# Kernel tuning notes

Hardware: AMD Instinct MI355X
Metric: run time of the kernel (lower is better)

The kernel has to match this reference:

```python
import jax, jax.numpy as jnp
import numpy as np

N, FIN, C1, C2 = 4096, 6, 1000, 1000
K1, K2, KR = 3, 6, 3
NR, S, NCLS = 20, 205, 40


def pairwise_adj(x):
    # exp(-squared_euclidean_distance), RGCNN pairwise_distance
    inner = -2.0 * jnp.einsum('bnf,bmf->bnm', x, x)
    sq = jnp.sum(x * x, axis=-1, keepdims=True)
    return jnp.exp(-(sq + inner + jnp.swapaxes(sq, 1, 2)))


def knn_sparsify(adj, k):
    # keep top-k similarities per row, zero the rest (get_one_matrix_knn)
    vals, idx = jax.lax.top_k(adj, k)
    B, n, _ = adj.shape
    b = jnp.arange(B)[:, None, None]
    r = jnp.arange(n)[None, :, None]
    return jnp.zeros_like(adj).at[b, r, idx].set(vals)


def get_laplacian(W):
    # normalized Laplacian L = I - D^-1/2 W D^-1/2
    dinv = 1.0 / jnp.sqrt(jnp.sum(W, axis=-1))
    Lnorm = W * dinv[:, :, None] * dinv[:, None, :]
    return jnp.eye(W.shape[-1], dtype=W.dtype)[None] - Lnorm


def cheb_conv(x, L, W, b, K):
    # Chebyshev recursion: Tx0=x, Tx1=Lx, Txk=2L Tx_{k-1} - Tx_{k-2}
    Tx = [x]
    if K > 1:
        Tx.append(jnp.einsum('bnm,bmf->bnf', L, x))
    for _ in range(2, K):
        Tx.append(2.0 * jnp.einsum('bnm,bmf->bnf', L, Tx[-1]) - Tx[-2])
    xhat = jnp.concatenate(Tx, axis=-1)  # [B, N, K*Fin]
    return jnp.einsum('bnf,fo->bno', xhat, W) + b


def setup_inputs() -> dict:
    key = jax.random.key(0)
    ks = jax.random.split(key, 16)
    sc = 0.02
    return {
        'x': jax.random.normal(ks[0], (1, N, FIN), jnp.float32),
        'k': 40,
        'batch_size': 1,
        'num_points': N,
        'vertices_Reeb': jax.random.normal(ks[1], (NR, 3), jnp.float32),
        'laplacian_Reeb': jax.random.normal(ks[2], (NR, NR), jnp.float32),
        'sccs': jax.random.randint(ks[3], (NR, S), 0, N),
        'W1': jax.random.normal(ks[4], (K1 * FIN, C1), jnp.float32) * sc,
        'b1': jnp.zeros((C1,), jnp.float32),
        'W2': jax.random.normal(ks[5], (K2 * C1, C2), jnp.float32) * sc,
        'b2': jnp.zeros((C2,), jnp.float32),
        'Wr': jax.random.normal(ks[6], (KR * C1, C2), jnp.float32) * sc,
        'br': jnp.zeros((C2,), jnp.float32),
        'fc1_w': jax.random.normal(ks[7], (2 * C2, 512), jnp.float32) * sc,
        'fc1_b': jnp.zeros((512,), jnp.float32),
        'fc2_w': jax.random.normal(ks[8], (512, 128), jnp.float32) * sc,
        'fc2_b': jnp.zeros((128,), jnp.float32),
        'fc3_w': jax.random.normal(ks[9], (128, NCLS), jnp.float32) * sc,
        'fc3_b': jnp.zeros((NCLS,), jnp.float32),
    }


def reference(x, k, batch_size, num_points, vertices_Reeb, laplacian_Reeb, sccs,
              W1, b1, W2, b2, Wr, br, fc1_w, fc1_b, fc2_w, fc2_b, fc3_w, fc3_b):
    fro = lambda a: jnp.linalg.norm(a.reshape(-1))
    regs = []
    # dynamic KNN graph + Laplacian (no_grad in original -> stop_gradient)
    L = jax.lax.stop_gradient(get_laplacian(knn_sparsify(pairwise_adj(x), k)))
    out = jax.nn.relu(cheb_conv(x, L, W1, b1, K1))  # [1, N, 1000]
    regs.append(fro(jnp.einsum('bnc,bnm,bmf->bcf', out, L, x)))
    # Reeb pooling: max over each scc's node features (sample 0)
    vfr = jnp.max(out[0][sccs], axis=1)[None]  # [1, 20, 1000]
    L_reeb = laplacian_Reeb[None]
    # second dynamic graph on features
    L2 = jax.lax.stop_gradient(get_laplacian(knn_sparsify(pairwise_adj(out), k)))
    out2 = jax.nn.relu(cheb_conv(out, L2, W2, b2, K2))
    regs.append(fro(jnp.einsum('bnc,bnm,bmf->bcf', out2, L2, x)))
    out_reeb = jax.nn.relu(cheb_conv(vfr, L_reeb, Wr, br, KR))
    out_m = jnp.max(out2, axis=1)       # [1, 1000]
    reeb_m = jnp.max(out_reeb, axis=1)  # [1, 1000]
    of = jnp.concatenate([reeb_m, out_m], axis=1)  # [1, 2000]
    of = jax.nn.relu(of @ fc1_w + fc1_b)
    regs += [jnp.linalg.norm(fc1_w.T[0]) ** 2, fc1_b[0] ** 2]
    of = jax.nn.relu(of @ fc2_w + fc2_b)
    regs += [jnp.linalg.norm(fc2_w.T[0]) ** 2, fc2_b[0] ** 2]
    of = of @ fc3_w + fc3_b  # [1, 40]
    regs += [jnp.linalg.norm(fc3_w.T[0]) ** 2, fc3_b[0] ** 2]
    return of, jnp.stack(regs)
```

## Files before the change

### kernel.cpp

```cpp
#include <hip/hip_runtime.h>
#include <math.h>

#define N4    4096
#define FDIM  6
#define CC    1000
#define KP    1024
#define KP6   (6 * KP)
#define KNN   40
#define NRB   20
#define SSC   205

typedef __attribute__((ext_vector_type(8))) short bf16x8;
typedef __attribute__((ext_vector_type(4))) float f32x4;

__device__ __forceinline__ unsigned short f2bf(float f) {
    unsigned u = __float_as_uint(f);
    u = (u + 0x7fffu + ((u >> 16) & 1u)) >> 16;
    return (unsigned short)u;
}
__device__ __forceinline__ float bf2f(short s) {
    return __uint_as_float(((unsigned)(unsigned short)s) << 16);
}

__device__ __forceinline__ unsigned d2key(float d) {
    unsigned u = __float_as_uint(d);
    return ((int)u < 0) ? u : (~u) ^ 0x80000000u;
}
__device__ __forceinline__ float key2d(unsigned k) {
    unsigned u = (k >> 31) ? k : (~k) ^ 0x80000000u;
    return __uint_as_float(u);
}

__device__ __forceinline__ void gload16(const unsigned short* g, short* l) {
    __builtin_amdgcn_global_load_lds(
        (const __attribute__((address_space(1))) unsigned int*)g,
        (__attribute__((address_space(3))) unsigned int*)l, 16, 0, 0);
}


__global__ __launch_bounds__(256) void sqx_kernel(const float* __restrict__ x,
                                                  float* __restrict__ sq1,
                                                  float* __restrict__ xhat) {
    int n = blockIdx.x * blockDim.x + threadIdx.x;
    if (n >= N4) return;
    float s = 0.f;
#pragma unroll
    for (int f = 0; f < FDIM; ++f) {
        float v = x[n * FDIM + f];
        s += v * v;
        xhat[n * 18 + f] = v;
    }
    sq1[n] = s;
}


#define NHC 8
#define HSTRIDE 257

struct TopkSh {
    unsigned sv[N4];
    int hist[NHC * HSTRIDE];
    int sc[256];
    float red[8];
    unsigned short cidx[N4];
    unsigned s_pfx;
    int s_need, s_cnt, s_m;
};

__device__ __forceinline__ void hist_pick(TopkSh& sh, int level, int t, int lane, int w, int nc) {
    if (t < 256) {
        int cnt = 0;
        for (int c = 0; c < nc; ++c) cnt += sh.hist[c * HSTRIDE + t];
        sh.sc[t] = cnt;
    }
    __syncthreads();
    if (w == 0) {
        int need = sh.s_need;
        unsigned pfx = sh.s_pfx;
        int c0 = sh.sc[4 * lane + 0], c1 = sh.sc[4 * lane + 1];
        int c2 = sh.sc[4 * lane + 2], c3 = sh.sc[4 * lane + 3];
        int s = c0 + c1 + c2 + c3;
        int suf = s;
#pragma unroll
        for (int off = 1; off < 64; off <<= 1) {
            int ov = __shfl_down(suf, off, 64);
            if (lane + off < 64) suf += ov;
        }
        int above = suf - s;
        int i3 = above + c3, i2 = i3 + c2, i1 = i2 + c1, i0 = i1 + c0;
        if (i3 >= need && i3 - c3 < need) { sh.s_need = need - (i3 - c3); sh.s_pfx = pfx | ((unsigned)(4 * lane + 3) << level); }
        if (i2 >= need && i2 - c2 < need) { sh.s_need = need - (i2 - c2); sh.s_pfx = pfx | ((unsigned)(4 * lane + 2) << level); }
        if (i1 >= need && i1 - c1 < need) { sh.s_need = need - (i1 - c1); sh.s_pfx = pfx | ((unsigned)(4 * lane + 1) << level); }
        if (i0 >= need && i0 - c0 < need) { sh.s_need = need - (i0 - c0); sh.s_pfx = pfx | ((unsigned)(4 * lane + 0) << level); }
    }
    __syncthreads();
}

__device__ void topk_select(TopkSh& sh, int n, int* __restrict__ idx,
                            float* __restrict__ val, float* __restrict__ rowsum) {
    int t = threadIdx.x, lane = t & 63, w = t >> 6;
    if (t == 0) { sh.s_pfx = 0u; sh.s_need = KNN; sh.s_cnt = 0; sh.s_m = 0; }
    for (int q = t; q < NHC * HSTRIDE; q += 512) sh.hist[q] = 0;
    __syncthreads();
    int* hw = &sh.hist[(t & 7) * HSTRIDE];

    {
        unsigned prevb = 0xFFFFFFFFu; int rl = 0;
        for (int i = t; i < N4; i += 512) {
            unsigned b = sh.sv[i] >> 24;
            if (b == prevb) ++rl;
            else { if (rl) atomicAdd(&hw[prevb], rl); prevb = b; rl = 1; }
        }
        if (rl) atomicAdd(&hw[prevb], rl);
    }
    __syncthreads();
    hist_pick(sh, 24, t, lane, w, NHC);
    unsigned b1 = sh.s_pfx >> 24;

    for (int i = t; i < N4; i += 512) {
        unsigned u = sh.sv[i];
        bool isc = ((u >> 24) >= b1);
        unsigned long long mm = __ballot(isc);
        int cw = __popcll(mm);
        int base = 0;
        if (lane == 0 && cw) base = atomicAdd(&sh.s_m, cw);
        base = __shfl(base, 0);
        if (isc) sh.cidx[base + __popcll(mm & ((1ull << lane) - 1ull))] = (unsigned short)i;
    }
    __syncthreads();
    int mcnt = sh.s_m;

    for (int level = 16; level >= 0; level -= 8) {
        for (int q = t; q < HSTRIDE; q += 512) sh.hist[q] = 0;
        __syncthreads();
        unsigned pfx = sh.s_pfx;
        for (int j = t; j < mcnt; j += 512) {
            unsigned u = sh.sv[sh.cidx[j]];
            if ((u >> (level + 8)) == (pfx >> (level + 8)))
                atomicAdd(&sh.hist[(u >> level) & 255], 1);
        }
        __syncthreads();
        hist_pick(sh, level, t, lane, w, 1);
    }
    unsigned Tbits = sh.s_pfx;
    float Tf = __expf(-key2d(Tbits));
    int needEq = sh.s_need;

    float psum = 0.f;
    for (int j = t; j < mcnt; j += 512) {
        unsigned u = sh.sv[sh.cidx[j]];
        if (u > Tbits) {
            int p = atomicAdd(&sh.s_cnt, 1);
            float v = __expf(-key2d(u));
            idx[(size_t)n * KNN + p] = (int)sh.cidx[j];
            val[(size_t)n * KNN + p] = v;
            psum += v;
        }
    }
#pragma unroll
    for (int o = 32; o; o >>= 1) psum += __shfl_down(psum, o);
    if (lane == 0) sh.red[w] = psum;
    __syncthreads();
    if (t == 0) {
        float s = 0.f;
#pragma unroll
        for (int q = 0; q < 8; ++q) s += sh.red[q];
        rowsum[n] = s + (float)needEq * Tf;
    }

    if (t < 64) {
        int filled = KNN - needEq;
        for (int ib = 0; ib < N4 && filled < KNN; ib += 64) {
            bool eq = (sh.sv[ib + t] == Tbits);
            unsigned long long m = __ballot(eq);
            int pre = __popcll(m & ((1ull << t) - 1ull));
            if (eq && (filled + pre) < KNN) {
                idx[(size_t)n * KNN + filled + pre] = ib + t;
                val[(size_t)n * KNN + filled + pre] = Tf;
            }
            filled += __popcll(m);
        }
    }
}

__global__ __launch_bounds__(512) void topk_fused1(const float* __restrict__ x,
                                                   const float* __restrict__ sq1,
                                                   int* __restrict__ idx, float* __restrict__ val,
                                                   float* __restrict__ rowsum) {
    __shared__ TopkSh sh;
    __shared__ float xn[FDIM];
    __shared__ float sns;
    int n = blockIdx.x;
    int t = threadIdx.x;
    if (t < FDIM) xn[t] = x[n * FDIM + t];
    if (t == FDIM) sns = sq1[n];
    __syncthreads();
    float x0 = xn[0], x1 = xn[1], x2 = xn[2], x3 = xn[3], x4 = xn[4], x5 = xn[5];
    float sn = sns;
    for (int i = t; i < N4; i += 512) {
        const float2* xi = (const float2*)(x + i * FDIM);
        float2 p0 = xi[0], p1 = xi[1], p2 = xi[2];
        float d = x0 * p0.x + x1 * p0.y + x2 * p1.x + x3 * p1.y + x4 * p2.x + x5 * p2.y;
        float e = sn + sq1[i] - 2.f * d;
        sh.sv[i] = d2key(e);
    }
    topk_select(sh, n, idx, val, rowsum);
}

__global__ __launch_bounds__(512) void topk_radix(const unsigned short* __restrict__ S,
                                                  int* __restrict__ idx, float* __restrict__ val,
                                                  float* __restrict__ rowsum) {
    __shared__ TopkSh sh;
    int n = blockIdx.x;
    int t = threadIdx.x;
    const unsigned short* row = S + (size_t)n * N4;
    bf16x8 a = *(const bf16x8*)(row + 8 * t);
#pragma unroll
    for (int q = 0; q < 8; ++q) sh.sv[8 * t + q] = d2key(bf2f(a[q]));
    topk_select(sh, n, idx, val, rowsum);
}

__global__ __launch_bounds__(256) void wnorm_kernel(float* __restrict__ wv,
                                                    const int* __restrict__ idx,
                                                    const float* __restrict__ rs) {
    int i = blockIdx.x * 256 + threadIdx.x;
    if (i >= N4 * KNN) return;
    int n = i / KNN;
    wv[i] = wv[i] * rsqrtf(rs[n]) * rsqrtf(rs[idx[i]]);
}

__global__ __launch_bounds__(64) void spmv_cheb(const float* __restrict__ Tc,
                                                const float* __restrict__ Tp,
                                                float* __restrict__ Tn,
                                                const int* __restrict__ idx,
                                                const float* __restrict__ wv,
                                                int F, int sC, int sP, int sN,
                                                float a, float b) {
    __shared__ int   si[KNN];
    __shared__ float sw[KNN];
    int n = blockIdx.x;
    if (threadIdx.x < KNN) {
        si[threadIdx.x] = idx[(size_t)n * KNN + threadIdx.x];
        sw[threadIdx.x] = wv[(size_t)n * KNN + threadIdx.x];
    }
    __syncthreads();
    for (int c = threadIdx.x; c < F; c += blockDim.x) {
        float s = 0.f;
#pragma unroll 8
        for (int j = 0; j < KNN; ++j) s += sw[j] * Tc[(size_t)si[j] * sC + c];
        float v = a * (Tc[(size_t)n * sC + c] - s);
        if (b != 0.f) v -= b * Tp[(size_t)n * sP + c];
        Tn[(size_t)n * sN + c] = v;
    }
}

__global__ __launch_bounds__(256) void spmv_cheb_bf(const unsigned short* __restrict__ Tcbf,
                                                    const unsigned short* __restrict__ Tpbf,
                                                    unsigned short* __restrict__ Tnbf,
                                                    const int* __restrict__ idx,
                                                    const float* __restrict__ wv,
                                                    float a, float b) {
    __shared__ int   si[KNN];
    __shared__ float sw[KNN];
    __shared__ float part[128][8];
    int n = blockIdx.x;
    int t = threadIdx.x;
    int tt = t & 127, h = t >> 7;
    if (t < KNN) {
        si[t] = idx[(size_t)n * KNN + t];
        sw[t] = wv[(size_t)n * KNN + t];
    }
    __syncthreads();
    int c = tt * 8;
    float acc0 = 0, acc1 = 0, acc2 = 0, acc3 = 0, acc4 = 0, acc5 = 0, acc6 = 0, acc7 = 0;
    int j0 = h * 20;
#pragma unroll 4
    for (int j = j0; j < j0 + 20; ++j) {
        bf16x8 v = *(const bf16x8*)(Tcbf + (size_t)si[j] * KP6 + c);
        float wj = sw[j];
        acc0 += wj * bf2f(v[0]); acc1 += wj * bf2f(v[1]);
        acc2 += wj * bf2f(v[2]); acc3 += wj * bf2f(v[3]);
        acc4 += wj * bf2f(v[4]); acc5 += wj * bf2f(v[5]);
        acc6 += wj * bf2f(v[6]); acc7 += wj * bf2f(v[7]);
    }
    if (h == 1) {
        part[tt][0] = acc0; part[tt][1] = acc1; part[tt][2] = acc2; part[tt][3] = acc3;
        part[tt][4] = acc4; part[tt][5] = acc5; part[tt][6] = acc6; part[tt][7] = acc7;
    }
    __syncthreads();
    if (h == 0) {
        acc0 += part[tt][0]; acc1 += part[tt][1]; acc2 += part[tt][2]; acc3 += part[tt][3];
        acc4 += part[tt][4]; acc5 += part[tt][5]; acc6 += part[tt][6]; acc7 += part[tt][7];
        bf16x8 tc = *(const bf16x8*)(Tcbf + (size_t)n * KP6 + c);
        float o0 = a * (bf2f(tc[0]) - acc0), o1 = a * (bf2f(tc[1]) - acc1);
        float o2 = a * (bf2f(tc[2]) - acc2), o3 = a * (bf2f(tc[3]) - acc3);
        float o4 = a * (bf2f(tc[4]) - acc4), o5 = a * (bf2f(tc[5]) - acc5);
        float o6 = a * (bf2f(tc[6]) - acc6), o7 = a * (bf2f(tc[7]) - acc7);
        if (b != 0.f) {
            bf16x8 tp = *(const bf16x8*)(Tpbf + (size_t)n * KP6 + c);
            o0 -= b * bf2f(tp[0]); o1 -= b * bf2f(tp[1]);
            o2 -= b * bf2f(tp[2]); o3 -= b * bf2f(tp[3]);
            o4 -= b * bf2f(tp[4]); o5 -= b * bf2f(tp[5]);
            o6 -= b * bf2f(tp[6]); o7 -= b * bf2f(tp[7]);
        }
        bf16x8 ob;
        ob[0] = (short)f2bf(o0); ob[1] = (short)f2bf(o1);
        ob[2] = (short)f2bf(o2); ob[3] = (short)f2bf(o3);
        ob[4] = (short)f2bf(o4); ob[5] = (short)f2bf(o5);
        ob[6] = (short)f2bf(o6); ob[7] = (short)f2bf(o7);
        *(bf16x8*)(Tnbf + (size_t)n * KP6 + c) = ob;
    }
}


__global__ __launch_bounds__(256) void cvt_bf16_kernel(const float* __restrict__ in,
                                                       unsigned short* __restrict__ out) {
    int i = blockIdx.x * 256 + threadIdx.x;
    int r = i >> 7, g = i & 127;
    bf16x8 v;
    if (g < 125) {
        float4 a = *(const float4*)(in + (size_t)r * CC + g * 8);
        float4 b = *(const float4*)(in + (size_t)r * CC + g * 8 + 4);
        v[0] = (short)f2bf(a.x); v[1] = (short)f2bf(a.y);
        v[2] = (short)f2bf(a.z); v[3] = (short)f2bf(a.w);
        v[4] = (short)f2bf(b.x); v[5] = (short)f2bf(b.y);
        v[6] = (short)f2bf(b.z); v[7] = (short)f2bf(b.w);
    } else {
#pragma unroll
        for (int q = 0; q < 8; ++q) v[q] = 0;
    }
    *(bf16x8*)(out + (size_t)r * KP6 + g * 8) = v;
}

__global__ __launch_bounds__(256) void w2t_kernel(const float* __restrict__ W2,
                                                  unsigned short* __restrict__ out) {
    __shared__ unsigned short tile[64][65];
    int t = threadIdx.x;
    int k0 = blockIdx.x * 64, n0 = blockIdx.y * 64, s = blockIdx.z;
#pragma unroll
    for (int p = 0; p < 16; ++p) {
        int i = p * 256 + t;
        int kk = i >> 6, nn = i & 63;
        int k = k0 + kk, n = n0 + nn;
        float v = (k < CC && n < CC) ? W2[((size_t)s * CC + k) * CC + n] : 0.f;
        tile[kk][nn] = f2bf(v);
    }
    __syncthreads();
#pragma unroll
    for (int p = 0; p < 16; ++p) {
        int i = p * 256 + t;
        int nn = i >> 6, kk = i & 63;
        out[(size_t)(n0 + nn) * KP6 + (size_t)s * KP + k0 + kk] = tile[kk][nn];
    }
}


#define LDT 32
#define SP2 136
#define SP 264
#define ABUF (128 * LDT)
#define BBUF (256 * LDT)

template<int STR>
__device__ __forceinline__ void gemm_core128_bk64(const unsigned short* __restrict__ Ag,
                                                  const unsigned short* __restrict__ Bg,
                                                  short* sm, int t,
                                                  int kbeg, int kend,
                                                  f32x4 (&acc)[4][4]) {
    int l = t & 63, w = t >> 6;
    int wm = (w >> 1) * 64, wn = (w & 1) * 64;
    int lr = l & 15, lq8 = (l >> 4) * 8;
    short* A0 = sm;
    short* A1 = sm + ABUF;
    short* B0 = sm + 2 * ABUF;
    short* B1 = sm + 3 * ABUF;
    size_t ga0 = (size_t)(32 * w + (l >> 2)) * STR + (l & 3) * 8;
    size_t ga1 = ga0 + (size_t)16 * STR;
    int lo = (32 * w) * LDT;
    for (int k0 = kbeg; k0 < kend; k0 += 64) {
        gload16(Ag + ga0 + k0,      A0 + lo);
        gload16(Ag + ga1 + k0,      A0 + lo + 16 * LDT);
        gload16(Ag + ga0 + k0 + 32, A1 + lo);
        gload16(Ag + ga1 + k0 + 32, A1 + lo + 16 * LDT);
        gload16(Bg + ga0 + k0,      B0 + lo);
        gload16(Bg + ga1 + k0,      B0 + lo + 16 * LDT);
        gload16(Bg + ga0 + k0 + 32, B1 + lo);
        gload16(Bg + ga1 + k0 + 32, B1 + lo + 16 * LDT);
        __syncthreads();
        bf16x8 af[4], bfr[4];
#pragma unroll
        for (int mi = 0; mi < 4; ++mi)
            af[mi] = *(const bf16x8*)&A0[(wm + mi * 16 + lr) * LDT + lq8];
#pragma unroll
        for (int ni = 0; ni < 4; ++ni)
            bfr[ni] = *(const bf16x8*)&B0[(wn + ni * 16 + lr) * LDT + lq8];
#pragma unroll
        for (int mi = 0; mi < 4; ++mi)
#pragma unroll
            for (int ni = 0; ni < 4; ++ni)
                acc[mi][ni] = __builtin_amdgcn_mfma_f32_16x16x32_bf16(af[mi], bfr[ni], acc[mi][ni], 0, 0, 0);
#pragma unroll
        for (int mi = 0; mi < 4; ++mi)
            af[mi] = *(const bf16x8*)&A1[(wm + mi * 16 + lr) * LDT + lq8];
#pragma unroll
        for (int ni = 0; ni < 4; ++ni)
            bfr[ni] = *(const bf16x8*)&B1[(wn + ni * 16 + lr) * LDT + lq8];
#pragma unroll
        for (int mi = 0; mi < 4; ++mi)
#pragma unroll
            for (int ni = 0; ni < 4; ++ni)
                acc[mi][ni] = __builtin_amdgcn_mfma_f32_16x16x32_bf16(af[mi], bfr[ni], acc[mi][ni], 0, 0, 0);
        __syncthreads();
    }
}

template<int STR>
__device__ __forceinline__ void gemm_core256(const unsigned short* __restrict__ Ag,
                                             const unsigned short* __restrict__ Bg,
                                             short* As, short* Bs, int t,
                                             int kbeg, int kend,
                                             f32x4 (&acc)[4][8]) {
    int l = t & 63, w = t >> 6;
    int wm = (w >> 1) * 64, wn = (w & 1) * 128;
    int lr = l & 15, lq8 = (l >> 4) * 8;
    size_t soff = (size_t)(16 * w + (l >> 2)) * STR + (l & 3) * 8;
    const unsigned short* gA = Ag + soff;
    const unsigned short* gB = Bg + soff;
    int wb = w * 512;
    gload16(gA + kbeg, As + wb);
    gload16(gA + kbeg + (size_t)64 * STR, As + wb + 64 * LDT);
    gload16(gB + kbeg, Bs + wb);
    gload16(gB + kbeg + (size_t)64 * STR, Bs + wb + 64 * LDT);
    gload16(gB + kbeg + (size_t)128 * STR, Bs + wb + 128 * LDT);
    gload16(gB + kbeg + (size_t)192 * STR, Bs + wb + 192 * LDT);
    __syncthreads();
    int cur = 0;
    for (int k0 = kbeg; k0 < kend; k0 += 32) {
        int nxt = cur ^ 1;
        if (k0 + 32 < kend) {
            short* nA = As + nxt * ABUF + wb;
            short* nB = Bs + nxt * BBUF + wb;
            gload16(gA + k0 + 32, nA);
            gload16(gA + k0 + 32 + (size_t)64 * STR, nA + 64 * LDT);
            gload16(gB + k0 + 32, nB);
            gload16(gB + k0 + 32 + (size_t)64 * STR, nB + 64 * LDT);
            gload16(gB + k0 + 32 + (size_t)128 * STR, nB + 128 * LDT);
            gload16(gB + k0 + 32 + (size_t)192 * STR, nB + 192 * LDT);
        }
        const short* cA = As + cur * ABUF;
        const short* cB = Bs + cur * BBUF;
        bf16x8 af[4], bfr[8];
#pragma unroll
        for (int mi = 0; mi < 4; ++mi)
            af[mi] = *(const bf16x8*)&cA[(wm + mi * 16 + lr) * LDT + lq8];
#pragma unroll
        for (int ni = 0; ni < 8; ++ni)
            bfr[ni] = *(const bf16x8*)&cB[(wn + ni * 16 + lr) * LDT + lq8];
#pragma unroll
        for (int mi = 0; mi < 4; ++mi)
#pragma unroll
            for (int ni = 0; ni < 8; ++ni)
                acc[mi][ni] = __builtin_amdgcn_mfma_f32_16x16x32_bf16(af[mi], bfr[ni], acc[mi][ni], 0, 0, 0);
        __syncthreads();
        cur = nxt;
    }
}

__global__ __launch_bounds__(256) void gemm_mfma_big(const unsigned short* __restrict__ A,
                                                     const unsigned short* __restrict__ B,
                                                     unsigned short* __restrict__ Cp) {
    __shared__ short smem[4 * ABUF];
    int t = threadIdx.x;
    int m0 = blockIdx.x * 128, n0 = blockIdx.y * 128;
    int kz = blockIdx.z;
    unsigned short* C = Cp + (size_t)kz * N4 * CC;
    f32x4 acc[4][4] = {};
    gemm_core128_bk64<KP6>(A + (size_t)m0 * KP6, B + (size_t)n0 * KP6, smem, t,
                           kz * 2 * KP, kz * 2 * KP + 2 * KP, acc);
    int l = t & 63, w = t >> 6;
    int wn = (w & 1) * 64;
    int lr = l & 15, lq4 = (l >> 4) * 4;
    int lrow = (w >> 1) * 16 + lq4;
#pragma unroll
    for (int mi = 0; mi < 4; ++mi) {
        __syncthreads();
#pragma unroll
        for (int ni = 0; ni < 4; ++ni) {
            int col = wn + ni * 16 + lr;
            f32x4 v = acc[mi][ni];
#pragma unroll
            for (int r = 0; r < 4; ++r) smem[(lrow + r) * SP2 + col] = (short)f2bf(v[r]);
        }
        __syncthreads();
#pragma unroll
        for (int q = 0; q < 2; ++q) {
            int row = q * 16 + (t >> 4);
            int col = (t & 15) * 8;
            int gm = m0 + (row >> 4) * 64 + mi * 16 + (row & 15);
            int gn = n0 + col;
            if (gn < CC) {
                bf16x8 vv = *(bf16x8*)&smem[row * SP2 + col];
                *(bf16x8*)(C + (size_t)gm * CC + gn) = vv;
            }
        }
    }
}

__global__ __launch_bounds__(256) void bias_relu_merge(const unsigned short* __restrict__ Cp,
                                                       const float* __restrict__ b2,
                                                       float* __restrict__ out2) {
    size_t i8 = (size_t)blockIdx.x * 256 + threadIdx.x;
    if (i8 >= (size_t)N4 * CC / 8) return;
    size_t i = i8 * 8;
    int c = (int)(i % CC);
    const size_t S = (size_t)N4 * CC;
    float s[8] = {};
#pragma unroll
    for (int z = 0; z < 3; ++z) {
        bf16x8 v = *(const bf16x8*)(Cp + z * S + i);
#pragma unroll
        for (int q = 0; q < 8; ++q) s[q] += bf2f(v[q]);
    }
    float4 o0, o1;
    o0.x = fmaxf(s[0] + b2[c + 0], 0.f); o0.y = fmaxf(s[1] + b2[c + 1], 0.f);
    o0.z = fmaxf(s[2] + b2[c + 2], 0.f); o0.w = fmaxf(s[3] + b2[c + 3], 0.f);
    o1.x = fmaxf(s[4] + b2[c + 4], 0.f); o1.y = fmaxf(s[5] + b2[c + 5], 0.f);
    o1.z = fmaxf(s[6] + b2[c + 6], 0.f); o1.w = fmaxf(s[7] + b2[c + 7], 0.f);
    *(float4*)(out2 + i) = o0;
    *(float4*)(out2 + i + 4) = o1;
}

__global__ __launch_bounds__(256, 2) void gram2_mfma(const unsigned short* __restrict__ Tall,
                                                     const float* __restrict__ sq2,
                                                     unsigned short* __restrict__ S) {
    __shared__ short smem[2 * ABUF + 2 * BBUF];
    short* As = smem;
    short* Bs = smem + 2 * ABUF;
    int t = threadIdx.x;
    int m0 = blockIdx.x * 128, n0 = blockIdx.y * 256;
    f32x4 acc[4][8] = {};
    gemm_core256<KP6>(Tall + (size_t)m0 * KP6, Tall + (size_t)n0 * KP6, As, Bs, t, 0, KP, acc);
    int l = t & 63, w = t >> 6;
    int wn = (w & 1) * 128;
    int lr = l & 15, lq4 = (l >> 4) * 4;
    int lrow = (w >> 1) * 16 + lq4;
#pragma unroll
    for (int mi = 0; mi < 4; ++mi) {
        __syncthreads();
        int mbase = m0 + (w >> 1) * 64 + mi * 16 + lq4;
#pragma unroll
        for (int ni = 0; ni < 8; ++ni) {
            int col = wn + ni * 16 + lr;
            float sn = sq2[n0 + col];
            f32x4 v = acc[mi][ni];
#pragma unroll
            for (int r = 0; r < 4; ++r)
                smem[(lrow + r) * SP + col] = (short)f2bf(sq2[mbase + r] + sn - 2.f * v[r]);
        }
        __syncthreads();
#pragma unroll
        for (int q = 0; q < 4; ++q) {
            int row = q * 8 + (t >> 5);
            int col = (t & 31) * 8;
            int gm = m0 + (row >> 4) * 64 + mi * 16 + (row & 15);
            int gn = n0 + col;
            bf16x8 vv = *(bf16x8*)&smem[row * SP + col];
            *(bf16x8*)(S + (size_t)gm * N4 + gn) = vv;
        }
    }
}


__global__ __launch_bounds__(256) void cheb1_out_kernel(const float* __restrict__ xhat,
                                                        const float* __restrict__ W1,
                                                        const float* __restrict__ b1,
                                                        float* __restrict__ outF) {
    __shared__ float xh[16][18];
    int n0 = blockIdx.x * 16;
    int tid = threadIdx.x;
    for (int i = tid; i < 16 * 18; i += 256) xh[i / 18][i % 18] = xhat[(size_t)n0 * 18 + i];
    __syncthreads();
    for (int c0 = 0; c0 < CC; c0 += 256) {
        int c = c0 + tid;
        if (c < CC) {
            float acc[16];
#pragma unroll
            for (int r = 0; r < 16; ++r) acc[r] = 0.f;
            for (int f = 0; f < 18; ++f) {
                float wv = W1[(size_t)f * CC + c];
#pragma unroll
                for (int r = 0; r < 16; ++r) acc[r] += xh[r][f] * wv;
            }
            float bb = b1[c];
#pragma unroll
            for (int r = 0; r < 16; ++r)
                outF[(size_t)(n0 + r) * CC + c] = fmaxf(acc[r] + bb, 0.f);
        }
    }
}


__global__ __launch_bounds__(256) void matT6_partial(const float* __restrict__ O,
                                                     const float* __restrict__ T, int ts,
                                                     float* __restrict__ M) {
    __shared__ float sT[128][6];
    int t = threadIdx.x;
    int c = blockIdx.x * 256 + t;
    int n0 = blockIdx.y * 128;
    for (int i = t; i < 128 * 6; i += 256) {
        int nn = i / 6, f = i % 6;
        sT[nn][f] = T[(size_t)(n0 + nn) * ts + f];
    }
    __syncthreads();
    if (c >= CC) return;
    float a0 = 0, a1 = 0, a2 = 0, a3 = 0, a4 = 0, a5 = 0;
    for (int nn = 0; nn < 128; ++nn) {
        float o = O[(size_t)(n0 + nn) * CC + c];
        a0 += o * sT[nn][0]; a1 += o * sT[nn][1]; a2 += o * sT[nn][2];
        a3 += o * sT[nn][3]; a4 += o * sT[nn][4]; a5 += o * sT[nn][5];
    }
    atomicAdd(&M[0 * CC + c], a0);
    atomicAdd(&M[1 * CC + c], a1);
    atomicAdd(&M[2 * CC + c], a2);
    atomicAdd(&M[3 * CC + c], a3);
    atomicAdd(&M[4 * CC + c], a4);
    atomicAdd(&M[5 * CC + c], a5);
}

__global__ __launch_bounds__(256) void fro_kernel(const float* __restrict__ M, float* __restrict__ dst) {
    __shared__ float red[256];
    int t = threadIdx.x;
    int i = blockIdx.x * 256 + t;
    float v = (i < 6 * CC) ? M[i] : 0.f;
    red[t] = v * v;
    __syncthreads();
    for (int o = 128; o; o >>= 1) { if (t < o) red[t] += red[t + o]; __syncthreads(); }
    if (t == 0) atomicAdd(dst, red[0]);
}


__global__ __launch_bounds__(256) void vfr_kernel(const float* __restrict__ outF,
                                                  const int* __restrict__ sccs,
                                                  float* __restrict__ vfr) {
    int r = blockIdx.y;
    int c = blockIdx.x * 256 + threadIdx.x;
    if (c >= CC) return;
    int s0 = blockIdx.z * 41;
    float m = 0.f;
    for (int s = s0; s < s0 + 41; ++s) {
        int n = sccs[r * SSC + s];
        m = fmaxf(m, outF[(size_t)n * CC + c]);
    }
    atomicMax((int*)&vfr[(size_t)r * CC + c], __float_as_int(m));
}

__global__ __launch_bounds__(256) void sq2_kernel(const float* __restrict__ outF,
                                                  float* __restrict__ sq2) {
    int lane = threadIdx.x & 63, w = threadIdx.x >> 6;
    int n = blockIdx.x * 4 + w;
    const float* row = outF + (size_t)n * CC;
    float s = 0.f;
    for (int i = lane; i < CC; i += 64) { float v = row[i]; s += v * v; }
#pragma unroll
    for (int o = 32; o; o >>= 1) s += __shfl_down(s, o);
    if (lane == 0) sq2[n] = s;
}

__global__ __launch_bounds__(256) void colmax_kernel(const float* __restrict__ O,
                                                     float* __restrict__ dst) {
    int c = blockIdx.x * 256 + threadIdx.x;
    if (c >= CC) return;
    int n0 = blockIdx.y * 64;
    float m = 0.f;
    for (int n = n0; n < n0 + 64; ++n) m = fmaxf(m, O[(size_t)n * CC + c]);
    atomicMax((int*)&dst[c], __float_as_int(m));
}


__global__ __launch_bounds__(256) void reeb_mm_kernel(const float* __restrict__ Lr,
                                                      const float* __restrict__ Vin,
                                                      const float* __restrict__ Vsub,
                                                      float* __restrict__ Vout, float a2) {
    int c = blockIdx.x * 256 + threadIdx.x;
    if (c >= CC) return;
    int r = blockIdx.y;
    float s = 0.f;
#pragma unroll
    for (int j = 0; j < NRB; ++j) s += Lr[r * NRB + j] * Vin[(size_t)j * CC + c];
    float v = a2 * s;
    if (Vsub) v -= Vsub[(size_t)r * CC + c];
    Vout[(size_t)r * CC + c] = v;
}

#define RKC 25
__global__ __launch_bounds__(256) void reeb_conv_splitk(const float* __restrict__ vfr,
                                                        const float* __restrict__ tr1,
                                                        const float* __restrict__ tr2,
                                                        const float* __restrict__ Wr,
                                                        float* __restrict__ rpre) {
    __shared__ float sA[NRB][RKC];
    int t = threadIdx.x;
    int kbase = blockIdx.y * RKC;
    for (int i = t; i < NRB * RKC; i += 256) {
        int r = i / RKC, kk = i % RKC;
        int kg = kbase + kk;
        float v;
        if (kg < CC)           v = vfr[(size_t)r * CC + kg];
        else if (kg < 2 * CC)  v = tr1[(size_t)r * CC + kg - CC];
        else                   v = tr2[(size_t)r * CC + kg - 2 * CC];
        sA[r][kk] = v;
    }
    __syncthreads();
    int c = blockIdx.x * 256 + t;
    if (c >= CC) return;
    float acc[NRB];
#pragma unroll
    for (int r = 0; r < NRB; ++r) acc[r] = 0.f;
    for (int kk = 0; kk < RKC; ++kk) {
        float wv = Wr[(size_t)(kbase + kk) * CC + c];
#pragma unroll
        for (int r = 0; r < NRB; ++r) acc[r] += sA[r][kk] * wv;
    }
#pragma unroll
    for (int r = 0; r < NRB; ++r) atomicAdd(&rpre[(size_t)r * CC + c], acc[r]);
}

__global__ __launch_bounds__(256) void reeb_max_kernel(const float* __restrict__ pre,
                                                       const float* __restrict__ br,
                                                       float* __restrict__ rbm) {
    int c = blockIdx.x * 256 + threadIdx.x;
    if (c >= CC) return;
    float bb = br[c];
    float m = 0.f;
    for (int r = 0; r < NRB; ++r) m = fmaxf(m, fmaxf(pre[(size_t)r * CC + c] + bb, 0.f));
    rbm[c] = m;
}


__global__ __launch_bounds__(256) void fc1_kernel(const float* __restrict__ rbm,
                                                  const float* __restrict__ otm,
                                                  const float* __restrict__ w,
                                                  float* __restrict__ h1pre) {
    int j = blockIdx.x * 256 + threadIdx.x;
    if (j >= 512) return;
    int i0 = blockIdx.y * 250;
    float s = 0.f;
    for (int i = i0; i < i0 + 250; ++i) {
        float v = (i < CC) ? rbm[i] : otm[i - CC];
        s += v * w[(size_t)i * 512 + j];
    }
    atomicAdd(&h1pre[j], s);
}

__global__ __launch_bounds__(512) void fc23_kernel(const float* __restrict__ h1pre,
                                                   const float* __restrict__ b1f,
                                                   const float* __restrict__ w2,
                                                   const float* __restrict__ b2f,
                                                   const float* __restrict__ w3,
                                                   const float* __restrict__ b3f,
                                                   float* __restrict__ dout) {
    __shared__ float h1[512];
    __shared__ float h2[128];
    int t = threadIdx.x;
    h1[t] = fmaxf(h1pre[t] + b1f[t], 0.f);
    __syncthreads();
    if (t < 128) {
        float s = b2f[t];
        for (int i = 0; i < 512; ++i) s += h1[i] * w2[(size_t)i * 128 + t];
        h2[t] = fmaxf(s, 0.f);
    }
    __syncthreads();
    if (t < 40) {
        float s = b3f[t];
        for (int i = 0; i < 128; ++i) s += h2[i] * w3[(size_t)i * 40 + t];
        dout[t] = s;
    }
}

__global__ __launch_bounds__(256) void finalize_kernel(const float* __restrict__ racc,
                                                       const float* __restrict__ f1w,
                                                       const float* __restrict__ f1b,
                                                       const float* __restrict__ f2w,
                                                       const float* __restrict__ f2b,
                                                       const float* __restrict__ f3w,
                                                       const float* __restrict__ f3b,
                                                       float* __restrict__ dout) {
    __shared__ float red[256];
    __shared__ float res[3];
    int t = threadIdx.x;
    float s1 = 0.f, s2 = 0.f, s3 = 0.f;
    for (int i = t; i < 2000; i += 256) { float v = f1w[(size_t)i * 512]; s1 += v * v; }
    for (int i = t; i < 512; i += 256) { float v = f2w[(size_t)i * 128]; s2 += v * v; }
    if (t < 128) { float v = f3w[(size_t)t * 40]; s3 = v * v; }

    red[t] = s1; __syncthreads();
    for (int o = 128; o; o >>= 1) { if (t < o) red[t] += red[t + o]; __syncthreads(); }
    if (t == 0) res[0] = red[0];
    __syncthreads();
    red[t] = s2; __syncthreads();
    for (int o = 128; o; o >>= 1) { if (t < o) red[t] += red[t + o]; __syncthreads(); }
    if (t == 0) res[1] = red[0];
    __syncthreads();
    red[t] = s3; __syncthreads();
    for (int o = 128; o; o >>= 1) { if (t < o) red[t] += red[t + o]; __syncthreads(); }
    if (t == 0) res[2] = red[0];
    __syncthreads();

    if (t == 0) {
        dout[40] = sqrtf(racc[0]);
        dout[41] = sqrtf(racc[1]);
        dout[42] = res[0];
        dout[43] = f1b[0] * f1b[0];
        dout[44] = res[1];
        dout[45] = f2b[0] * f2b[0];
        dout[46] = res[2];
        dout[47] = f3b[0] * f3b[0];
    }
}


extern "C" void kernel_launch(void* const* d_in, const int* in_sizes, int n_in,
                              void* d_out, int out_size, void* d_ws, size_t ws_size,
                              hipStream_t stream) {
    const float* x    = (const float*)d_in[0];
    const float* Lr   = (const float*)d_in[5];
    const int*   sccs = (const int*)d_in[6];
    const float* W1   = (const float*)d_in[7];
    const float* b1   = (const float*)d_in[8];
    const float* W2   = (const float*)d_in[9];
    const float* b2   = (const float*)d_in[10];
    const float* Wr   = (const float*)d_in[11];
    const float* br   = (const float*)d_in[12];
    const float* f1w  = (const float*)d_in[13];
    const float* f1b  = (const float*)d_in[14];
    const float* f2w  = (const float*)d_in[15];
    const float* f2b  = (const float*)d_in[16];
    const float* f3w  = (const float*)d_in[17];
    const float* f3b  = (const float*)d_in[18];
    float* dout = (float*)d_out;

    char* ws = (char*)d_ws;
    size_t off = 0;
    auto alloc = [&](size_t bytes) -> char* {
        char* p = ws + off;
        off = (off + bytes + 255) & ~(size_t)255;
        return p;
    };
    float* outF = (float*)alloc((size_t)N4 * CC * 4);
    unsigned short* Cpb = (unsigned short*)alloc((size_t)6 * N4 * CC * 2);
    unsigned short* Sb  = (unsigned short*)alloc((size_t)N4 * N4 * 2);
    unsigned short* Tall = (unsigned short*)alloc((size_t)N4 * KP6 * 2);
    unsigned short* W2T6 = Sb;
    float* xhat = (float*)alloc((size_t)N4 * 18 * 4);
    float* sq1  = (float*)alloc(N4 * 4);
    float* sq2  = (float*)alloc(N4 * 4);
    float* rs1  = (float*)alloc(N4 * 4);
    float* rs2  = (float*)alloc(N4 * 4);
    float* wv1  = (float*)alloc((size_t)N4 * KNN * 4);
    float* wv2  = (float*)alloc((size_t)N4 * KNN * 4);
    int*   ix1  = (int*)alloc((size_t)N4 * KNN * 4);
    int*   ix2  = (int*)alloc((size_t)N4 * KNN * 4);
    float* t2x  = (float*)alloc((size_t)N4 * FDIM * 4);
    float* tr1  = (float*)alloc((size_t)NRB * CC * 4);
    float* tr2  = (float*)alloc((size_t)NRB * CC * 4);
    char*  zbase = ws + off;
    float* Mb   = (float*)alloc(6 * CC * 4);
    float* Mb2  = (float*)alloc(6 * CC * 4);
    float* rbm  = (float*)alloc(CC * 4);
    float* otm  = (float*)alloc(CC * 4);
    float* h1p  = (float*)alloc(512 * 4);
    float* racc = (float*)alloc(64 * 4);
    float* rpre = (float*)alloc((size_t)NRB * CC * 4);
    float* vfr  = (float*)alloc((size_t)NRB * CC * 4);
    size_t zlen = (size_t)((ws + off) - zbase);
    if (off > ws_size) return;

    hipMemsetAsync(zbase, 0, zlen, stream);

    sqx_kernel<<<(N4 + 255) / 256, 256, 0, stream>>>(x, sq1, xhat);
    topk_fused1<<<N4, 512, 0, stream>>>(x, sq1, ix1, wv1, rs1);
    wnorm_kernel<<<(N4 * KNN + 255) / 256, 256, 0, stream>>>(wv1, ix1, rs1);

    spmv_cheb<<<N4, 64, 0, stream>>>(xhat, xhat, xhat + 6, ix1, wv1, FDIM, 18, 18, 18, 1.f, 0.f);
    spmv_cheb<<<N4, 64, 0, stream>>>(xhat + 6, xhat, xhat + 12, ix1, wv1, FDIM, 18, 18, 18, 2.f, 1.f);
    cheb1_out_kernel<<<N4 / 16, 256, 0, stream>>>(xhat, W1, b1, outF);

    matT6_partial<<<dim3(4, 32), 256, 0, stream>>>(outF, xhat + 6, 18, Mb);
    fro_kernel<<<24, 256, 0, stream>>>(Mb, racc + 0);

    vfr_kernel<<<dim3(4, NRB, 5), 256, 0, stream>>>(outF, sccs, vfr);

    sq2_kernel<<<N4 / 4, 256, 0, stream>>>(outF, sq2);
    cvt_bf16_kernel<<<N4 * 128 / 256, 256, 0, stream>>>(outF, Tall);
    gram2_mfma<<<dim3(N4 / 128, N4 / 256), 256, 0, stream>>>(Tall, sq2, Sb);
    topk_radix<<<N4, 512, 0, stream>>>(Sb, ix2, wv2, rs2);
    wnorm_kernel<<<(N4 * KNN + 255) / 256, 256, 0, stream>>>(wv2, ix2, rs2);

    w2t_kernel<<<dim3(16, 16, 6), 256, 0, stream>>>(W2, W2T6);

    spmv_cheb<<<N4, 64, 0, stream>>>(x, x, t2x, ix2, wv2, FDIM, FDIM, FDIM, FDIM, 1.f, 0.f);

    spmv_cheb_bf<<<N4, 256, 0, stream>>>(Tall + 0 * KP, Tall + 0 * KP, Tall + 1 * KP, ix2, wv2, 1.f, 0.f);
    spmv_cheb_bf<<<N4, 256, 0, stream>>>(Tall + 1 * KP, Tall + 0 * KP, Tall + 2 * KP, ix2, wv2, 2.f, 1.f);
    spmv_cheb_bf<<<N4, 256, 0, stream>>>(Tall + 2 * KP, Tall + 1 * KP, Tall + 3 * KP, ix2, wv2, 2.f, 1.f);
    spmv_cheb_bf<<<N4, 256, 0, stream>>>(Tall + 3 * KP, Tall + 2 * KP, Tall + 4 * KP, ix2, wv2, 2.f, 1.f);
    spmv_cheb_bf<<<N4, 256, 0, stream>>>(Tall + 4 * KP, Tall + 3 * KP, Tall + 5 * KP, ix2, wv2, 2.f, 1.f);

    gemm_mfma_big<<<dim3(N4 / 128, 8, 3), 256, 0, stream>>>(Tall, W2T6, Cpb);
    bias_relu_merge<<<(int)(((size_t)N4 * CC / 8 + 255) / 256), 256, 0, stream>>>(Cpb, b2, outF);

    matT6_partial<<<dim3(4, 32), 256, 0, stream>>>(outF, t2x, FDIM, Mb2);
    fro_kernel<<<24, 256, 0, stream>>>(Mb2, racc + 1);

    colmax_kernel<<<dim3(4, 64), 256, 0, stream>>>(outF, otm);

    reeb_mm_kernel<<<dim3(4, NRB), 256, 0, stream>>>(Lr, vfr, nullptr, tr1, 1.f);
    reeb_mm_kernel<<<dim3(4, NRB), 256, 0, stream>>>(Lr, tr1, vfr, tr2, 2.f);
    reeb_conv_splitk<<<dim3(4, 120), 256, 0, stream>>>(vfr, tr1, tr2, Wr, rpre);
    reeb_max_kernel<<<4, 256, 0, stream>>>(rpre, br, rbm);

    fc1_kernel<<<dim3(2, 8), 256, 0, stream>>>(rbm, otm, f1w, h1p);
    fc23_kernel<<<1, 512, 0, stream>>>(h1p, f1b, f2w, f2b, f3w, f3b, dout);
    finalize_kernel<<<1, 256, 0, stream>>>(racc, f1w, f1b, f2w, f2b, f3w, f3b, dout);
}
```

Measured before the change: 665.6 us.

## Fuse top-k histogram into key generation, skip low radix pass, split SpMV columns

The top-k kernels now build the first radix histogram while writing the keys, which removes a separate pass over shared memory. The bf16 path stops the radix refinement at bit 16, because the low 16 bits of bf16-derived keys carry no information, and fills the threshold bits to match. The bf16 Chebyshev SpMV now splits the feature columns across two blocks in y and the neighbours across four warp groups, with a padded partial-sum buffer, giving more parallelism per row. The risk is extra reduction overhead and subtle threshold-tie correctness in the skipped level.

```diff
diff --git a/kernel.cpp b/kernel.cpp
--- a/kernel.cpp
+++ b/kernel.cpp
@@ -67,6 +67,11 @@
     int s_need, s_cnt, s_m;
 };
 
+__device__ __forceinline__ void topk_prep(TopkSh& sh, int t) {
+    if (t == 0) { sh.s_pfx = 0u; sh.s_need = KNN; sh.s_cnt = 0; sh.s_m = 0; }
+    for (int q = t; q < NHC * HSTRIDE; q += 512) sh.hist[q] = 0;
+}
+
 __device__ __forceinline__ void hist_pick(TopkSh& sh, int level, int t, int lane, int w, int nc) {
     if (t < 256) {
         int cnt = 0;
@@ -96,23 +101,10 @@
     __syncthreads();
 }
 
-__device__ void topk_select(TopkSh& sh, int n, int* __restrict__ idx,
-                            float* __restrict__ val, float* __restrict__ rowsum) {
+template<int LASTLEVEL>
+__device__ void topk_core(TopkSh& sh, int n, int* __restrict__ idx,
+                          float* __restrict__ val, float* __restrict__ rowsum) {
     int t = threadIdx.x, lane = t & 63, w = t >> 6;
-    if (t == 0) { sh.s_pfx = 0u; sh.s_need = KNN; sh.s_cnt = 0; sh.s_m = 0; }
-    for (int q = t; q < NHC * HSTRIDE; q += 512) sh.hist[q] = 0;
-    __syncthreads();
-    int* hw = &sh.hist[(t & 7) * HSTRIDE];
-
-    {
-        unsigned prevb = 0xFFFFFFFFu; int rl = 0;
-        for (int i = t; i < N4; i += 512) {
-            unsigned b = sh.sv[i] >> 24;
-            if (b == prevb) ++rl;
-            else { if (rl) atomicAdd(&hw[prevb], rl); prevb = b; rl = 1; }
-        }
-        if (rl) atomicAdd(&hw[prevb], rl);
-    }
     __syncthreads();
     hist_pick(sh, 24, t, lane, w, NHC);
     unsigned b1 = sh.s_pfx >> 24;
@@ -130,7 +122,7 @@
     __syncthreads();
     int mcnt = sh.s_m;
 
-    for (int level = 16; level >= 0; level -= 8) {
+    for (int level = 16; level >= LASTLEVEL; level -= 8) {
         for (int q = t; q < HSTRIDE; q += 512) sh.hist[q] = 0;
         __syncthreads();
         unsigned pfx = sh.s_pfx;
@@ -143,6 +135,7 @@
         hist_pick(sh, level, t, lane, w, 1);
     }
     unsigned Tbits = sh.s_pfx;
+    if (LASTLEVEL == 16) Tbits |= (Tbits & 0x80000000u) ? 0u : 0xFFFFu;
     float Tf = __expf(-key2d(Tbits));
     int needEq = sh.s_need;
 
@@ -194,17 +187,21 @@
     int t = threadIdx.x;
     if (t < FDIM) xn[t] = x[n * FDIM + t];
     if (t == FDIM) sns = sq1[n];
+    topk_prep(sh, t);
     __syncthreads();
     float x0 = xn[0], x1 = xn[1], x2 = xn[2], x3 = xn[3], x4 = xn[4], x5 = xn[5];
     float sn = sns;
+    int* hw = &sh.hist[(t & 7) * HSTRIDE];
     for (int i = t; i < N4; i += 512) {
         const float2* xi = (const float2*)(x + i * FDIM);
         float2 p0 = xi[0], p1 = xi[1], p2 = xi[2];
         float d = x0 * p0.x + x1 * p0.y + x2 * p1.x + x3 * p1.y + x4 * p2.x + x5 * p2.y;
         float e = sn + sq1[i] - 2.f * d;
-        sh.sv[i] = d2key(e);
-    }
-    topk_select(sh, n, idx, val, rowsum);
+        unsigned k = d2key(e);
+        sh.sv[i] = k;
+        atomicAdd(&hw[k >> 24], 1);
+    }
+    topk_core<0>(sh, n, idx, val, rowsum);
 }
 
 __global__ __launch_bounds__(512) void topk_radix(const unsigned short* __restrict__ S,
@@ -213,11 +210,18 @@
     __shared__ TopkSh sh;
     int n = blockIdx.x;
     int t = threadIdx.x;
+    topk_prep(sh, t);
     const unsigned short* row = S + (size_t)n * N4;
     bf16x8 a = *(const bf16x8*)(row + 8 * t);
-#pragma unroll
-    for (int q = 0; q < 8; ++q) sh.sv[8 * t + q] = d2key(bf2f(a[q]));
-    topk_select(sh, n, idx, val, rowsum);
+    __syncthreads();
+    int* hw = &sh.hist[(t & 7) * HSTRIDE];
+#pragma unroll
+    for (int q = 0; q < 8; ++q) {
+        unsigned k = d2key(bf2f(a[q]));
+        sh.sv[8 * t + q] = k;
+        atomicAdd(&hw[k >> 24], 1);
+    }
+    topk_core<16>(sh, n, idx, val, rowsum);
 }
 
 __global__ __launch_bounds__(256) void wnorm_kernel(float* __restrict__ wv,
@@ -262,20 +266,20 @@
                                                     float a, float b) {
     __shared__ int   si[KNN];
     __shared__ float sw[KNN];
-    __shared__ float part[128][8];
+    __shared__ float part[3][64][9];
     int n = blockIdx.x;
     int t = threadIdx.x;
-    int tt = t & 127, h = t >> 7;
+    int tt = t & 63, g = t >> 6;
     if (t < KNN) {
         si[t] = idx[(size_t)n * KNN + t];
         sw[t] = wv[(size_t)n * KNN + t];
     }
     __syncthreads();
-    int c = tt * 8;
+    int c = blockIdx.y * 512 + tt * 8;
     float acc0 = 0, acc1 = 0, acc2 = 0, acc3 = 0, acc4 = 0, acc5 = 0, acc6 = 0, acc7 = 0;
-    int j0 = h * 20;
-#pragma unroll 4
-    for (int j = j0; j < j0 + 20; ++j) {
+    int j0 = g * 10;
+#pragma unroll
+    for (int j = j0; j < j0 + 10; ++j) {
         bf16x8 v = *(const bf16x8*)(Tcbf + (size_t)si[j] * KP6 + c);
         float wj = sw[j];
         acc0 += wj * bf2f(v[0]); acc1 += wj * bf2f(v[1]);
@@ -283,14 +287,19 @@
         acc4 += wj * bf2f(v[4]); acc5 += wj * bf2f(v[5]);
         acc6 += wj * bf2f(v[6]); acc7 += wj * bf2f(v[7]);
     }
-    if (h == 1) {
-        part[tt][0] = acc0; part[tt][1] = acc1; part[tt][2] = acc2; part[tt][3] = acc3;
-        part[tt][4] = acc4; part[tt][5] = acc5; part[tt][6] = acc6; part[tt][7] = acc7;
-    }
-    __syncthreads();
-    if (h == 0) {
-        acc0 += part[tt][0]; acc1 += part[tt][1]; acc2 += part[tt][2]; acc3 += part[tt][3];
-        acc4 += part[tt][4]; acc5 += part[tt][5]; acc6 += part[tt][6]; acc7 += part[tt][7];
+    if (g) {
+        float* p = part[g - 1][tt];
+        p[0] = acc0; p[1] = acc1; p[2] = acc2; p[3] = acc3;
+        p[4] = acc4; p[5] = acc5; p[6] = acc6; p[7] = acc7;
+    }
+    __syncthreads();
+    if (g == 0) {
+#pragma unroll
+        for (int pg = 0; pg < 3; ++pg) {
+            const float* p = part[pg][tt];
+            acc0 += p[0]; acc1 += p[1]; acc2 += p[2]; acc3 += p[3];
+            acc4 += p[4]; acc5 += p[5]; acc6 += p[6]; acc7 += p[7];
+        }
         bf16x8 tc = *(const bf16x8*)(Tcbf + (size_t)n * KP6 + c);
         float o0 = a * (bf2f(tc[0]) - acc0), o1 = a * (bf2f(tc[1]) - acc1);
         float o2 = a * (bf2f(tc[2]) - acc2), o3 = a * (bf2f(tc[3]) - acc3);
@@ -900,11 +909,11 @@
 
     spmv_cheb<<<N4, 64, 0, stream>>>(x, x, t2x, ix2, wv2, FDIM, FDIM, FDIM, FDIM, 1.f, 0.f);
 
-    spmv_cheb_bf<<<N4, 256, 0, stream>>>(Tall + 0 * KP, Tall + 0 * KP, Tall + 1 * KP, ix2, wv2, 1.f, 0.f);
-    spmv_cheb_bf<<<N4, 256, 0, stream>>>(Tall + 1 * KP, Tall + 0 * KP, Tall + 2 * KP, ix2, wv2, 2.f, 1.f);
-    spmv_cheb_bf<<<N4, 256, 0, stream>>>(Tall + 2 * KP, Tall + 1 * KP, Tall + 3 * KP, ix2, wv2, 2.f, 1.f);
-    spmv_cheb_bf<<<N4, 256, 0, stream>>>(Tall + 3 * KP, Tall + 2 * KP, Tall + 4 * KP, ix2, wv2, 2.f, 1.f);
-    spmv_cheb_bf<<<N4, 256, 0, stream>>>(Tall + 4 * KP, Tall + 3 * KP, Tall + 5 * KP, ix2, wv2, 2.f, 1.f);
+    spmv_cheb_bf<<<dim3(N4, 2), 256, 0, stream>>>(Tall + 0 * KP, Tall + 0 * KP, Tall + 1 * KP, ix2, wv2, 1.f, 0.f);
+    spmv_cheb_bf<<<dim3(N4, 2), 256, 0, stream>>>(Tall + 1 * KP, Tall + 0 * KP, Tall + 2 * KP, ix2, wv2, 2.f, 1.f);
+    spmv_cheb_bf<<<dim3(N4, 2), 256, 0, stream>>>(Tall + 2 * KP, Tall + 1 * KP, Tall + 3 * KP, ix2, wv2, 2.f, 1.f);
+    spmv_cheb_bf<<<dim3(N4, 2), 256, 0, stream>>>(Tall + 3 * KP, Tall + 2 * KP, Tall + 4 * KP, ix2, wv2, 2.f, 1.f);
+    spmv_cheb_bf<<<dim3(N4, 2), 256, 0, stream>>>(Tall + 4 * KP, Tall + 3 * KP, Tall + 5 * KP, ix2, wv2, 2.f, 1.f);
 
     gemm_mfma_big<<<dim3(N4 / 128, 8, 3), 256, 0, stream>>>(Tall, W2T6, Cpb);
     bias_relu_merge<<<(int)(((size_t)N4 * CC / 8 + 255) / 256), 256, 0, stream>>>(Cpb, b2, outF);
```

After: 627.7 us. 5.7% less time.
